# Kernel tuning notes

Hardware: AMD Instinct MI355X
Metric: run time of the kernel (lower is better)

Reference implementation:

```python
import jax, jax.numpy as jnp
import numpy as np

N_NODES = 50000
N_EDGES = 1250000
VOCAB = 50000
EMBED = 64
HIDDEN = 64
NUM_REL = 3
N_CLASSES = 2
N_GRAPHS = 512


def setup_inputs() -> dict:
    key = jax.random.key(0)
    ks = jax.random.split(key, 12)
    x = jax.random.randint(ks[0], (N_NODES,), 0, VOCAB, dtype=jnp.int32)
    edge_index = jax.random.randint(ks[1], (2, N_EDGES), 0, N_NODES, dtype=jnp.int32)
    edge_type = jax.random.randint(ks[2], (N_EDGES,), 0, NUM_REL, dtype=jnp.int32)
    batch = jnp.sort(jax.random.randint(ks[3], (N_NODES,), 0, N_GRAPHS, dtype=jnp.int32))
    s = 0.05
    emb = jax.random.normal(ks[4], (VOCAB, EMBED), jnp.float32) * s
    w1_rel = jax.random.normal(ks[5], (NUM_REL, EMBED, HIDDEN), jnp.float32) * s
    w1_root = jax.random.normal(ks[6], (EMBED, HIDDEN), jnp.float32) * s
    b1 = jnp.zeros((HIDDEN,), jnp.float32)
    w2_rel = jax.random.normal(ks[7], (NUM_REL, HIDDEN, HIDDEN), jnp.float32) * s
    w2_root = jax.random.normal(ks[8], (HIDDEN, HIDDEN), jnp.float32) * s
    b2 = jnp.zeros((HIDDEN,), jnp.float32)
    lin_w = jax.random.normal(ks[9], (HIDDEN, N_CLASSES), jnp.float32) * s
    lin_b = jnp.zeros((N_CLASSES,), jnp.float32)
    return {"x": x, "edge_index": edge_index, "edge_type": edge_type, "batch": batch,
            "emb": emb, "w1_rel": w1_rel, "w1_root": w1_root, "b1": b1,
            "w2_rel": w2_rel, "w2_root": w2_root, "b2": b2,
            "lin_w": lin_w, "lin_b": lin_b}


def rgcn_conv(h, src, dst, edge_type, w_rel, w_root, bias):
    # PyG RGCNConv: out = h @ W_root + bias + sum_r mean-aggregated (h_src @ W_r)
    out = h @ w_root + bias
    h_src = h[src]  # [E, F] gather
    for r in range(NUM_REL):
        mask = (edge_type == r).astype(h.dtype)  # [E]
        m = (h_src @ w_rel[r]) * mask[:, None]   # [E, H]
        s = jax.ops.segment_sum(m, dst, num_segments=N_NODES)
        cnt = jax.ops.segment_sum(mask, dst, num_segments=N_NODES)
        out = out + s / jnp.maximum(cnt, 1.0)[:, None]
    return out


def reference(x, edge_index, edge_type, batch, emb, w1_rel, w1_root, b1,
              w2_rel, w2_root, b2, lin_w, lin_b):
    src, dst = edge_index[0], edge_index[1]
    emb_eff = emb.at[0].set(0.0)  # padding_idx=0
    h = emb_eff[x]  # [N, EMBED]
    h = jax.nn.relu(rgcn_conv(h, src, dst, edge_type, w1_rel, w1_root, b1))
    h = jax.nn.relu(rgcn_conv(h, src, dst, edge_type, w2_rel, w2_root, b2))
    # global mean pool over graphs
    sums = jax.ops.segment_sum(h, batch, num_segments=N_GRAPHS)
    cnt = jax.ops.segment_sum(jnp.ones((h.shape[0],), h.dtype), batch, num_segments=N_GRAPHS)
    pooled = sums / jnp.maximum(cnt, 1.0)[:, None]  # [G, HIDDEN]
    return pooled @ lin_w + lin_b  # [G, N_CLASSES]
```

## Files before the change

kernel.cpp:

```cpp
#include <hip/hip_runtime.h>

#define CHUNK 2048

__global__ __launch_bounds__(256) void embed_count_kernel(
    const int* __restrict__ x, const float* __restrict__ emb, float* __restrict__ h0,
    const int* __restrict__ ei, int* __restrict__ pcount,
    int n_nodes, int n_edges, int n_bkt, int embed_blocks)
{
    __shared__ int cnt[512];
    int t = threadIdx.x;
    if ((int)blockIdx.x < embed_blocks) {
        int tt = blockIdx.x * 256 + t;
        if (tt < n_nodes * 16) {
            int n = tt >> 4, q = tt & 15;
            int xv = x[n];
            float4 v = {0.f, 0.f, 0.f, 0.f};
            if (xv != 0) v = *(const float4*)(emb + (size_t)xv * 64 + q * 4);
            *(float4*)(h0 + (size_t)n * 64 + q * 4) = v;
        }
        return;
    }
    int jb = blockIdx.x - embed_blocks;
    for (int b = t; b < 512; b += 256) cnt[b] = 0;
    __syncthreads();
    int base = jb * CHUNK;
#pragma unroll
    for (int i = 0; i < CHUNK / 256; ++i) {
        int e = base + i * 256 + t;
        if (e < n_edges) atomicAdd(&cnt[ei[n_edges + e] >> 7], 1);
    }
    __syncthreads();
    for (int b = t; b < n_bkt; b += 256) pcount[jb * n_bkt + b] = cnt[b];
}

__global__ __launch_bounds__(256) void colscan_kernel(
    const int* __restrict__ pcount, int* __restrict__ pre,
    int* __restrict__ totals, int n_chk, int n_bkt)
{
    __shared__ int ps[256];
    int b = blockIdx.x, t = threadIdx.x;
    int v[4], s = 0;
#pragma unroll
    for (int i = 0; i < 4; ++i) {
        int jj = t * 4 + i;
        v[i] = (jj < n_chk) ? pcount[jj * n_bkt + b] : 0;
        s += v[i];
    }
    ps[t] = s;
    __syncthreads();
    for (int o = 1; o < 256; o <<= 1) {
        int u = (t >= o) ? ps[t - o] : 0;
        __syncthreads();
        ps[t] += u;
        __syncthreads();
    }
    int run = (t > 0) ? ps[t - 1] : 0;
#pragma unroll
    for (int i = 0; i < 4; ++i) {
        int jj = t * 4 + i;
        if (jj < n_chk) pre[jj * n_bkt + b] = run;
        run += v[i];
    }
    if (t == 255) totals[b] = run;
}

__global__ __launch_bounds__(512) void scan_buckets_kernel(
    const int* __restrict__ totals, int* __restrict__ bucket_start,
    int* __restrict__ rowstartR, int n_bkt, int n_edges, int n_nodes)
{
    __shared__ int part[512];
    int t = threadIdx.x;
    part[t] = (t < n_bkt) ? totals[t] : 0;
    __syncthreads();
    for (int off = 1; off < 512; off <<= 1) {
        int v = (t >= off) ? part[t - off] : 0;
        __syncthreads();
        part[t] += v;
        __syncthreads();
    }
    if (t == 0) { bucket_start[0] = 0; rowstartR[4 * n_nodes] = n_edges; }
    if (t < n_bkt) bucket_start[t + 1] = part[t];
}

__global__ __launch_bounds__(256) void scatter_kernel(
    const int* __restrict__ ei, const int* __restrict__ et,
    const int* __restrict__ pre, const int* __restrict__ bucket_start,
    int* __restrict__ esort, int n_edges, int n_bkt)
{
    __shared__ int myb[512], fill2[512];
    int t = threadIdx.x, j = blockIdx.x;
    for (int b = t; b < 512; b += 256) {
        myb[b] = (b < n_bkt) ? (bucket_start[b] + pre[j * n_bkt + b]) : 0;
        fill2[b] = 0;
    }
    __syncthreads();
    int base = j * CHUNK;
#pragma unroll
    for (int i = 0; i < CHUNK / 256; ++i) {
        int e = base + i * 256 + t;
        if (e < n_edges) {
            int s = ei[e], d = ei[n_edges + e], r = et[e];
            int b = d >> 7;
            int pos = myb[b] + atomicAdd(&fill2[b], 1);
            esort[pos] = s | (r << 16) | ((d & 127) << 18);
        }
    }
}

__global__ __launch_bounds__(256) void bucket_sort_kernel(
    const int* __restrict__ bucket_start, int* __restrict__ esort,
    int* __restrict__ scratch, int* __restrict__ rowstartR, int n_nodes)
{
    __shared__ int cnt[512], off[512], fill[512], ps[256];
    int t = threadIdx.x, b = blockIdx.x;
    int s = bucket_start[b], e = bucket_start[b + 1];
    cnt[t] = 0; cnt[t + 256] = 0; fill[t] = 0; fill[t + 256] = 0;
    __syncthreads();
    int* scr = scratch + (size_t)b * 8192;
    for (int i = s + t; i < e; i += 256) {
        int p = esort[i];
        scr[i - s] = p;
        atomicAdd(&cnt[(p >> 16) & 0x1FF], 1);
    }
    __syncthreads();
    int a0 = cnt[2 * t], a1 = cnt[2 * t + 1];
    ps[t] = a0 + a1;
    __syncthreads();
    for (int o = 1; o < 256; o <<= 1) {
        int v = (t >= o) ? ps[t - o] : 0;
        __syncthreads();
        ps[t] += v;
        __syncthreads();
    }
    int basex = (t > 0) ? ps[t - 1] : 0;
    off[2 * t] = basex;
    off[2 * t + 1] = basex + a0;
    __syncthreads();
    int d0 = b * 128 + (2 * t >> 2);
    if (d0 < n_nodes) rowstartR[b * 512 + 2 * t] = s + off[2 * t];
    int d1 = b * 128 + ((2 * t + 1) >> 2);
    if (d1 < n_nodes) rowstartR[b * 512 + 2 * t + 1] = s + off[2 * t + 1];
    __syncthreads();
    for (int i = s + t; i < e; i += 256) {
        int p = scr[i - s];
        int bin = (p >> 16) & 0x1FF;
        int pos = s + off[bin] + atomicAdd(&fill[bin], 1);
        esort[pos] = p;
    }
}

__global__ __launch_bounds__(256) void agg_kernel(
    const float* __restrict__ hin, const int* __restrict__ rowstartR,
    const int* __restrict__ esort, float* __restrict__ means, int n_nodes)
{
    int wid = (blockIdx.x * 256 + threadIdx.x) >> 6;
    int lane = threadIdx.x & 63;
    if (wid >= n_nodes) return;
    int q = lane >> 4;
    int c = lane & 15;
    int4 rs = *(const int4*)(rowstartR + wid * 4);

#pragma unroll
    for (int r = 0; r < 3; ++r) {
        int sR = (r == 0) ? rs.x : (r == 1) ? rs.y : rs.z;
        int eR = (r == 0) ? rs.y : (r == 1) ? rs.z : rs.w;
        float4 a = {0.f, 0.f, 0.f, 0.f};
        for (int i = sR + q; i < eR; i += 4) {
            int p = esort[i];
            float4 v = *(const float4*)(hin + (size_t)(p & 0xFFFF) * 64 + c * 4);
            a.x += v.x; a.y += v.y; a.z += v.z; a.w += v.w;
        }
        a.x += __shfl_xor(a.x, 16); a.y += __shfl_xor(a.y, 16);
        a.z += __shfl_xor(a.z, 16); a.w += __shfl_xor(a.w, 16);
        a.x += __shfl_xor(a.x, 32); a.y += __shfl_xor(a.y, 32);
        a.z += __shfl_xor(a.z, 32); a.w += __shfl_xor(a.w, 32);
        if (q == r) {
            float inv = 1.f / (float)max(eR - sR, 1);
            float4 m = {a.x * inv, a.y * inv, a.z * inv, a.w * inv};
            *(float4*)(means + (size_t)wid * 192 + r * 64 + c * 4) = m;
        }
    }
}

__global__ __launch_bounds__(256) void transform_kernel(
    const float* __restrict__ hin, const float* __restrict__ means,
    const float* __restrict__ wroot, const float* __restrict__ wrel,
    const float* __restrict__ bias, float* __restrict__ hout, int n_nodes)
{
    __shared__ float wsh[2][4096];
    int t = threadIdx.x;
    int gt = blockIdx.x * 256 + t;
    int g = gt >> 4, q = gt & 15;
    int n0 = g * 4;
    bool active = (n0 < n_nodes);

    {
        const float4* sp = (const float4*)wroot;
        float4* d = (float4*)wsh[0];
#pragma unroll
        for (int i = 0; i < 4; ++i) d[t + i * 256] = sp[t + i * 256];
    }

    float4 acc[4];
    float4 b = {0.f, 0.f, 0.f, 0.f};
    if (active) b = *(const float4*)(bias + q * 4);
#pragma unroll
    for (int i = 0; i < 4; ++i) acc[i] = b;

    const float* hv = hin + (size_t)n0 * 64;
    const float* mv = means + (size_t)n0 * 192;

    for (int s = 0; s < 4; ++s) {
        __syncthreads();
        if (s < 3) {
            const float4* sp = (const float4*)wrel + (size_t)s * 1024;
            float4* d = (float4*)wsh[(s + 1) & 1];
#pragma unroll
            for (int i = 0; i < 4; ++i) d[t + i * 256] = sp[t + i * 256];
        }
        const float* vbase = (s == 0) ? hv : (mv + (s - 1) * 64);
        int vstride = (s == 0) ? 64 : 192;
        const float* wbuf = wsh[s & 1];
        if (active) {
#pragma unroll 4
            for (int k4 = 0; k4 < 16; ++k4) {
                float4 v[4];
#pragma unroll
                for (int i = 0; i < 4; ++i)
                    v[i] = *(const float4*)(vbase + i * vstride + k4 * 4);
#pragma unroll
                for (int kk = 0; kk < 4; ++kk) {
                    float4 w = *(const float4*)(wbuf + (k4 * 4 + kk) * 64 + q * 4);
#pragma unroll
                    for (int i = 0; i < 4; ++i) {
                        float sv = kk == 0 ? v[i].x : kk == 1 ? v[i].y : kk == 2 ? v[i].z : v[i].w;
                        acc[i].x = fmaf(sv, w.x, acc[i].x);
                        acc[i].y = fmaf(sv, w.y, acc[i].y);
                        acc[i].z = fmaf(sv, w.z, acc[i].z);
                        acc[i].w = fmaf(sv, w.w, acc[i].w);
                    }
                }
            }
        }
    }
    if (active) {
        float* o = hout + (size_t)n0 * 64 + q * 4;
#pragma unroll
        for (int i = 0; i < 4; ++i) {
            float4 r = {fmaxf(acc[i].x, 0.f), fmaxf(acc[i].y, 0.f),
                        fmaxf(acc[i].z, 0.f), fmaxf(acc[i].w, 0.f)};
            *(float4*)(o + i * 64) = r;
        }
    }
}

__global__ __launch_bounds__(256) void pool_kernel(
    const float* __restrict__ h2, const int* __restrict__ batch,
    const float* __restrict__ linw, const float* __restrict__ linb,
    float* __restrict__ out, int n_nodes, int n_graphs)
{
    int wid = (blockIdx.x * 256 + threadIdx.x) >> 6;
    int lane = threadIdx.x & 63;
    if (wid >= n_graphs) return;
    int g = wid;
    int lo = 0, hi = n_nodes;
    while (lo < hi) { int mid = (lo + hi) >> 1; if (batch[mid] < g) lo = mid + 1; else hi = mid; }
    int s = lo;
    lo = 0; hi = n_nodes;
    while (lo < hi) { int mid = (lo + hi) >> 1; if (batch[mid] < g + 1) lo = mid + 1; else hi = mid; }
    int e = lo;
    float sum = 0.f;
    for (int n = s; n < e; ++n) sum += h2[(size_t)n * 64 + lane];
    float mean = sum / (float)max(e - s, 1);
    float d0 = mean * linw[lane * 2 + 0];
    float d1 = mean * linw[lane * 2 + 1];
    for (int off = 32; off > 0; off >>= 1) {
        d0 += __shfl_down(d0, off);
        d1 += __shfl_down(d1, off);
    }
    if (lane == 0) {
        out[g * 2 + 0] = d0 + linb[0];
        out[g * 2 + 1] = d1 + linb[1];
    }
}

extern "C" void kernel_launch(void* const* d_in, const int* in_sizes, int n_in,
                              void* d_out, int out_size, void* d_ws, size_t ws_size,
                              hipStream_t stream)
{
    const int*   x      = (const int*)d_in[0];
    const int*   ei     = (const int*)d_in[1];
    const int*   et     = (const int*)d_in[2];
    const int*   batch  = (const int*)d_in[3];
    const float* emb    = (const float*)d_in[4];
    const float* w1rel  = (const float*)d_in[5];
    const float* w1root = (const float*)d_in[6];
    const float* b1     = (const float*)d_in[7];
    const float* w2rel  = (const float*)d_in[8];
    const float* w2root = (const float*)d_in[9];
    const float* b2     = (const float*)d_in[10];
    const float* linw   = (const float*)d_in[11];
    const float* linb   = (const float*)d_in[12];
    float* out = (float*)d_out;

    const int N = in_sizes[0];
    const int E = in_sizes[2];
    const int G = out_size / 2;
    const int NBKT = (N + 127) >> 7;
    const int NCHK = (E + CHUNK - 1) / CHUNK;

    float* hA        = (float*)d_ws;
    float* hB        = hA + (size_t)N * 64;
    float* means     = hB + (size_t)N * 64;
    int*   esort     = (int*)(means + (size_t)N * 192);
    int*   rowstartR = esort + E;
    int*   bucket_start = rowstartR + 4 * N + 4;
    int*   totals    = bucket_start + NBKT + 1;
    int*   pcount    = (int*)means + 4 * 1024 * 1024;
    int*   pre       = (int*)means + 5 * 1024 * 1024;

    int embedBlocks = (N * 16 + 255) / 256;
    embed_count_kernel<<<embedBlocks + NCHK, 256, 0, stream>>>(
        x, emb, hA, ei, pcount, N, E, NBKT, embedBlocks);
    colscan_kernel<<<NBKT, 256, 0, stream>>>(pcount, pre, totals, NCHK, NBKT);
    scan_buckets_kernel<<<1, 512, 0, stream>>>(totals, bucket_start, rowstartR, NBKT, E, N);
    scatter_kernel<<<NCHK, 256, 0, stream>>>(ei, et, pre, bucket_start, esort, E, NBKT);
    bucket_sort_kernel<<<NBKT, 256, 0, stream>>>(bucket_start, esort, (int*)means, rowstartR, N);

    int aggBlocks = (N * 64 + 255) / 256;
    int tfBlocks  = ((N + 3) / 4 * 16 + 255) / 256;
    agg_kernel<<<aggBlocks, 256, 0, stream>>>(hA, rowstartR, esort, means, N);
    transform_kernel<<<tfBlocks, 256, 0, stream>>>(hA, means, w1root, w1rel, b1, hB, N);
    agg_kernel<<<aggBlocks, 256, 0, stream>>>(hB, rowstartR, esort, means, N);
    transform_kernel<<<tfBlocks, 256, 0, stream>>>(hB, means, w2root, w2rel, b2, hA, N);

    pool_kernel<<<(G * 64 + 255) / 256, 256, 0, stream>>>(hA, batch, linw, linb, out, N, G);
}
```

Measured before the change: 349.1 us.

## Fold bucket scan into scatter kernel and unroll agg edge loop by two

Removes the single-block scan_buckets launch: each scatter block now redundantly scans the bucket totals in shared memory, block 0 writes bucket_start, and colscan writes the rowstartR sentinel. This eliminates one kernel launch and its serialization point at the cost of repeated small scans per block. Separately, the aggregation loop processes two edges per lane-group iteration with two accumulators to raise memory-level parallelism on the gathers.

```diff
diff --git a/kernel.cpp b/kernel.cpp
--- a/kernel.cpp
+++ b/kernel.cpp
@@ -35,10 +35,12 @@
 
 __global__ __launch_bounds__(256) void colscan_kernel(
     const int* __restrict__ pcount, int* __restrict__ pre,
-    int* __restrict__ totals, int n_chk, int n_bkt)
+    int* __restrict__ totals, int* __restrict__ rowstartR,
+    int n_chk, int n_bkt, int n_edges, int n_nodes)
 {
     __shared__ int ps[256];
     int b = blockIdx.x, t = threadIdx.x;
+    if (b == 0 && t == 0) rowstartR[4 * n_nodes] = n_edges;
     int v[4], s = 0;
 #pragma unroll
     for (int i = 0; i < 4; ++i) {
@@ -64,35 +66,34 @@
     if (t == 255) totals[b] = run;
 }
 
-__global__ __launch_bounds__(512) void scan_buckets_kernel(
-    const int* __restrict__ totals, int* __restrict__ bucket_start,
-    int* __restrict__ rowstartR, int n_bkt, int n_edges, int n_nodes)
-{
-    __shared__ int part[512];
-    int t = threadIdx.x;
-    part[t] = (t < n_bkt) ? totals[t] : 0;
-    __syncthreads();
-    for (int off = 1; off < 512; off <<= 1) {
-        int v = (t >= off) ? part[t - off] : 0;
-        __syncthreads();
-        part[t] += v;
-        __syncthreads();
-    }
-    if (t == 0) { bucket_start[0] = 0; rowstartR[4 * n_nodes] = n_edges; }
-    if (t < n_bkt) bucket_start[t + 1] = part[t];
-}
-
 __global__ __launch_bounds__(256) void scatter_kernel(
     const int* __restrict__ ei, const int* __restrict__ et,
-    const int* __restrict__ pre, const int* __restrict__ bucket_start,
-    int* __restrict__ esort, int n_edges, int n_bkt)
-{
-    __shared__ int myb[512], fill2[512];
+    const int* __restrict__ pre, const int* __restrict__ totals,
+    int* __restrict__ esort, int* __restrict__ bucket_start,
+    int n_edges, int n_bkt)
+{
+    __shared__ int bs[512], fill2[512], ps[256];
     int t = threadIdx.x, j = blockIdx.x;
-    for (int b = t; b < 512; b += 256) {
-        myb[b] = (b < n_bkt) ? (bucket_start[b] + pre[j * n_bkt + b]) : 0;
-        fill2[b] = 0;
-    }
+    int a0 = (2 * t < n_bkt) ? totals[2 * t] : 0;
+    int a1 = (2 * t + 1 < n_bkt) ? totals[2 * t + 1] : 0;
+    ps[t] = a0 + a1;
+    __syncthreads();
+    for (int o = 1; o < 256; o <<= 1) {
+        int u = (t >= o) ? ps[t - o] : 0;
+        __syncthreads();
+        ps[t] += u;
+        __syncthreads();
+    }
+    int basex = (t > 0) ? ps[t - 1] : 0;
+    bs[2 * t] = basex;
+    bs[2 * t + 1] = basex + a0;
+    fill2[t] = 0; fill2[t + 256] = 0;
+    __syncthreads();
+    if (j == 0) {
+        for (int b = t; b < n_bkt; b += 256) bucket_start[b] = bs[b];
+        if (t == 0) bucket_start[n_bkt] = n_edges;
+    }
+    for (int b = t; b < n_bkt; b += 256) bs[b] += pre[j * n_bkt + b];
     __syncthreads();
     int base = j * CHUNK;
 #pragma unroll
@@ -101,7 +102,7 @@
         if (e < n_edges) {
             int s = ei[e], d = ei[n_edges + e], r = et[e];
             int b = d >> 7;
-            int pos = myb[b] + atomicAdd(&fill2[b], 1);
+            int pos = bs[b] + atomicAdd(&fill2[b], 1);
             esort[pos] = s | (r << 16) | ((d & 127) << 18);
         }
     }
@@ -165,11 +166,22 @@
         int sR = (r == 0) ? rs.x : (r == 1) ? rs.y : rs.z;
         int eR = (r == 0) ? rs.y : (r == 1) ? rs.z : rs.w;
         float4 a = {0.f, 0.f, 0.f, 0.f};
-        for (int i = sR + q; i < eR; i += 4) {
-            int p = esort[i];
-            float4 v = *(const float4*)(hin + (size_t)(p & 0xFFFF) * 64 + c * 4);
-            a.x += v.x; a.y += v.y; a.z += v.z; a.w += v.w;
-        }
+        float4 b = {0.f, 0.f, 0.f, 0.f};
+        int i = sR + 2 * q;
+        for (; i + 2 <= eR; i += 8) {
+            int p0 = esort[i];
+            int p1 = esort[i + 1];
+            float4 v0 = *(const float4*)(hin + (size_t)(p0 & 0xFFFF) * 64 + c * 4);
+            float4 v1 = *(const float4*)(hin + (size_t)(p1 & 0xFFFF) * 64 + c * 4);
+            a.x += v0.x; a.y += v0.y; a.z += v0.z; a.w += v0.w;
+            b.x += v1.x; b.y += v1.y; b.z += v1.z; b.w += v1.w;
+        }
+        if (i < eR) {
+            int p0 = esort[i];
+            float4 v0 = *(const float4*)(hin + (size_t)(p0 & 0xFFFF) * 64 + c * 4);
+            a.x += v0.x; a.y += v0.y; a.z += v0.z; a.w += v0.w;
+        }
+        a.x += b.x; a.y += b.y; a.z += b.z; a.w += b.w;
         a.x += __shfl_xor(a.x, 16); a.y += __shfl_xor(a.y, 16);
         a.z += __shfl_xor(a.z, 16); a.w += __shfl_xor(a.w, 16);
         a.x += __shfl_xor(a.x, 32); a.y += __shfl_xor(a.y, 32);
@@ -316,16 +328,16 @@
     int*   rowstartR = esort + E;
     int*   bucket_start = rowstartR + 4 * N + 4;
     int*   totals    = bucket_start + NBKT + 1;
+    int*   scratch   = (int*)means;
     int*   pcount    = (int*)means + 4 * 1024 * 1024;
     int*   pre       = (int*)means + 5 * 1024 * 1024;
 
     int embedBlocks = (N * 16 + 255) / 256;
     embed_count_kernel<<<embedBlocks + NCHK, 256, 0, stream>>>(
         x, emb, hA, ei, pcount, N, E, NBKT, embedBlocks);
-    colscan_kernel<<<NBKT, 256, 0, stream>>>(pcount, pre, totals, NCHK, NBKT);
-    scan_buckets_kernel<<<1, 512, 0, stream>>>(totals, bucket_start, rowstartR, NBKT, E, N);
-    scatter_kernel<<<NCHK, 256, 0, stream>>>(ei, et, pre, bucket_start, esort, E, NBKT);
-    bucket_sort_kernel<<<NBKT, 256, 0, stream>>>(bucket_start, esort, (int*)means, rowstartR, N);
+    colscan_kernel<<<NBKT, 256, 0, stream>>>(pcount, pre, totals, rowstartR, NCHK, NBKT, E, N);
+    scatter_kernel<<<NCHK, 256, 0, stream>>>(ei, et, pre, totals, esort, bucket_start, E, NBKT);
+    bucket_sort_kernel<<<NBKT, 256, 0, stream>>>(bucket_start, esort, scratch, rowstartR, N);
 
     int aggBlocks = (N * 64 + 255) / 256;
     int tfBlocks  = ((N + 3) / 4 * 16 + 255) / 256;
```

Result: faster. 339.7 us (-2.7%).
